# Kernel optimization log

Hardware: AMD Instinct MI355X
Metric: run time of the kernel (lower is better)

Reference implementation:

```python
import jax, jax.numpy as jnp
import numpy as np

EMBED_DIM = 2048
NUM_HEADS = 16
HEAD_DIM = EMBED_DIM // NUM_HEADS


def setup_inputs() -> dict:
    key = jax.random.key(0)
    ks = jax.random.split(key, 9)
    s = 1.0 / np.sqrt(EMBED_DIM)
    x = jax.random.normal(ks[0], (2, 2048, EMBED_DIM), dtype=jnp.float32)
    Wq = jax.random.uniform(ks[1], (EMBED_DIM, EMBED_DIM), jnp.float32, -s, s)
    bq = jax.random.uniform(ks[2], (EMBED_DIM,), jnp.float32, -s, s)
    Wk = jax.random.uniform(ks[3], (EMBED_DIM, EMBED_DIM), jnp.float32, -s, s)
    bk = jax.random.uniform(ks[4], (EMBED_DIM,), jnp.float32, -s, s)
    Wv = jax.random.uniform(ks[5], (EMBED_DIM, EMBED_DIM), jnp.float32, -s, s)
    bv = jax.random.uniform(ks[6], (EMBED_DIM,), jnp.float32, -s, s)
    Wo = jax.random.uniform(ks[7], (EMBED_DIM, EMBED_DIM), jnp.float32, -s, s)
    bo = jax.random.uniform(ks[8], (EMBED_DIM,), jnp.float32, -s, s)
    return {"x": x, "Wq": Wq, "bq": bq, "Wk": Wk, "bk": bk,
            "Wv": Wv, "bv": bv, "Wo": Wo, "bo": bo}


def reference(x, Wq, bq, Wk, bk, Wv, bv, Wo, bo):
    B, S, E = x.shape
    H, D = NUM_HEADS, HEAD_DIM
    # projections (torch Linear: y = x @ W.T + b)
    def proj(W, b):
        return (x @ W.T + b).reshape(B, S, H, D).transpose(0, 2, 1, 3)  # [B,H,S,D]
    q, k, v = proj(Wq, bq), proj(Wk, bk), proj(Wv, bv)
    scores = jnp.einsum('bhqd,bhkd->bhqk', q, k) / np.sqrt(D).astype(np.float32)
    causal = jnp.triu(jnp.ones((S, S), dtype=bool), k=1)
    scores = jnp.where(causal, jnp.float32(-1e9), scores)
    attn = jax.nn.softmax(scores, axis=-1)
    ctx = jnp.einsum('bhqk,bhkd->bhqd', attn, v)
    ctx = ctx.transpose(0, 2, 1, 3).reshape(B, S, E)
    return ctx @ Wo.T + bo
```

## Files before the change

### kernel.cpp

```cpp
#include <hip/hip_runtime.h>
#include <hip/hip_bf16.h>

typedef __bf16 bf16_t;
typedef bf16_t bf16x8 __attribute__((ext_vector_type(8)));
typedef float f32x4 __attribute__((ext_vector_type(4)));

__device__ __forceinline__ f32x4 mfma16(bf16x8 a, bf16x8 b, f32x4 c) {
    return __builtin_amdgcn_mfma_f32_16x16x32_bf16(a, b, c, 0, 0, 0);
}

__device__ __forceinline__ void load16_to_lds(const void* g, void* l) {
    __builtin_amdgcn_global_load_lds(
        (__attribute__((address_space(1))) unsigned int*)g,
        (__attribute__((address_space(3))) unsigned int*)l, 16, 0, 0);
}

__device__ __forceinline__ bf16x8 cvt8(f32x4 a, f32x4 b) {
    bf16x8 r;
    r[0] = (bf16_t)a[0]; r[1] = (bf16_t)a[1]; r[2] = (bf16_t)a[2]; r[3] = (bf16_t)a[3];
    r[4] = (bf16_t)b[0]; r[5] = (bf16_t)b[1]; r[6] = (bf16_t)b[2]; r[7] = (bf16_t)b[3];
    return r;
}

__global__ __launch_bounds__(256)
void cvt_bf16(const float* __restrict__ in, bf16_t* __restrict__ out) {
    const long i = ((long)blockIdx.x * 256 + threadIdx.x) * 8;
    *(bf16x8*)(out + i) = cvt8(*(const f32x4*)(in + i), *(const f32x4*)(in + i + 4));
}

__global__ __launch_bounds__(256)
void cvt_all(const float* __restrict__ x,
             const float* __restrict__ Wq, const float* __restrict__ Wk, const float* __restrict__ Wv,
             bf16_t* __restrict__ xb, bf16_t* __restrict__ wqb,
             bf16_t* __restrict__ wkb, bf16_t* __restrict__ wvb) {
    const long NW = 4194304;
    const int y = blockIdx.y;
    const float* s; bf16_t* o;
    if      (y == 0) { s = x;      o = xb;      }
    else if (y == 1) { s = x + NW; o = xb + NW; }
    else if (y == 2) { s = Wq;     o = wqb;     }
    else if (y == 3) { s = Wk;     o = wkb;     }
    else             { s = Wv;     o = wvb;     }
    const long i = ((long)blockIdx.x * 256 + threadIdx.x) * 8;
    *(bf16x8*)(o + i) = cvt8(*(const f32x4*)(s + i), *(const f32x4*)(s + i + 4));
}

__global__ __launch_bounds__(256)
void gemm_qkv(const bf16_t* __restrict__ X,
              const bf16_t* __restrict__ W0, const bf16_t* __restrict__ W1, const bf16_t* __restrict__ W2,
              const float* __restrict__ B0, const float* __restrict__ B1, const float* __restrict__ B2,
              bf16_t* __restrict__ O0, bf16_t* __restrict__ O1, bf16_t* __restrict__ O2)
{
    __shared__ __align__(16) bf16_t As[128 * 32];
    __shared__ __align__(16) bf16_t Bs[128 * 32];
    const int z = blockIdx.z;
    const bf16_t* W = (z == 0) ? W0 : (z == 1 ? W1 : W2);
    const float* Bv = (z == 0) ? B0 : (z == 1 ? B1 : B2);
    bf16_t* O       = (z == 0) ? O0 : (z == 1 ? O1 : O2);

    const int tid = threadIdx.x;
    const int w = tid >> 6, l = tid & 63;
    const int lm = l & 15, lq = l >> 4;
    const long arow0 = (long)blockIdx.y * 128;
    const long brow0 = (long)blockIdx.x * 128;
    const int wm = (w >> 1) * 64, wn = (w & 1) * 64;

    f32x4 acc[4][4] = {};

    for (int kt = 0; kt < 2048; kt += 32) {
#pragma unroll
        for (int i = 0; i < 2; ++i) {
            const int c = w * 128 + i * 64 + l;
            const int row = c >> 2, ce = (c & 3) * 8;
            load16_to_lds(X + (arow0 + row) * 2048 + kt + ce, As + (w * 2 + i) * 512);
            load16_to_lds(W + (brow0 + row) * 2048 + kt + ce, Bs + (w * 2 + i) * 512);
        }
        __syncthreads();
        bf16x8 af[4], bfr[4];
#pragma unroll
        for (int i = 0; i < 4; ++i)
            af[i] = *(const bf16x8*)(As + (wm + i * 16 + lm) * 32 + lq * 8);
#pragma unroll
        for (int j = 0; j < 4; ++j)
            bfr[j] = *(const bf16x8*)(Bs + (wn + j * 16 + lm) * 32 + lq * 8);
#pragma unroll
        for (int i = 0; i < 4; ++i)
#pragma unroll
            for (int j = 0; j < 4; ++j)
                acc[i][j] = mfma16(af[i], bfr[j], acc[i][j]);
        __syncthreads();
    }

    const float scale = (z == 0) ? 0.08838834764831845f : 1.0f;
#pragma unroll
    for (int j = 0; j < 4; ++j) {
        const int col = (int)brow0 + wn + j * 16 + lm;
        const float bb = Bv[col];
        const int h = col >> 7, d = col & 127;
#pragma unroll
        for (int i = 0; i < 4; ++i) {
            const int rbase = (int)arow0 + wm + i * 16 + lq * 4;
#pragma unroll
            for (int r = 0; r < 4; ++r) {
                const int row = rbase + r;
                const int b = row >> 11, s = row & 2047;
                const float v = (acc[i][j][r] + bb) * scale;
                long idx;
                if (z == 2) idx = ((long)(b * 16 + h) * 128 + d) * 2048 + s;
                else        idx = ((long)(b * 16 + h) * 2048 + s) * 128 + d;
                O[idx] = (bf16_t)v;
            }
        }
    }
}

__global__ __launch_bounds__(256)
void gemm_out(const bf16_t* __restrict__ A, const bf16_t* __restrict__ W,
              const float* __restrict__ Bv, float* __restrict__ O)
{
    __shared__ __align__(16) bf16_t As[128 * 32];
    __shared__ __align__(16) bf16_t Bs[128 * 32];

    const int tid = threadIdx.x;
    const int w = tid >> 6, l = tid & 63;
    const int lm = l & 15, lq = l >> 4;
    const long arow0 = (long)blockIdx.y * 128;
    const long brow0 = (long)blockIdx.x * 128;
    const int wm = (w >> 1) * 64, wn = (w & 1) * 64;

    f32x4 acc[4][4] = {};

    for (int kt = 0; kt < 2048; kt += 32) {
#pragma unroll
        for (int i = 0; i < 2; ++i) {
            const int c = w * 128 + i * 64 + l;
            const int row = c >> 2, ce = (c & 3) * 8;
            load16_to_lds(A + (arow0 + row) * 2048 + kt + ce, As + (w * 2 + i) * 512);
            load16_to_lds(W + (brow0 + row) * 2048 + kt + ce, Bs + (w * 2 + i) * 512);
        }
        __syncthreads();
        bf16x8 af[4], bfr[4];
#pragma unroll
        for (int i = 0; i < 4; ++i)
            af[i] = *(const bf16x8*)(As + (wm + i * 16 + lm) * 32 + lq * 8);
#pragma unroll
        for (int j = 0; j < 4; ++j)
            bfr[j] = *(const bf16x8*)(Bs + (wn + j * 16 + lm) * 32 + lq * 8);
#pragma unroll
        for (int i = 0; i < 4; ++i)
#pragma unroll
            for (int j = 0; j < 4; ++j)
                acc[i][j] = mfma16(af[i], bfr[j], acc[i][j]);
        __syncthreads();
    }

#pragma unroll
    for (int j = 0; j < 4; ++j) {
        const int col = (int)brow0 + wn + j * 16 + lm;
        const float bb = Bv[col];
#pragma unroll
        for (int i = 0; i < 4; ++i) {
            const int rbase = (int)arow0 + wm + i * 16 + lq * 4;
#pragma unroll
            for (int r = 0; r < 4; ++r)
                O[(long)(rbase + r) * 2048 + col] = acc[i][j][r] + bb;
        }
    }
}

__global__ __launch_bounds__(256, 4)
void attn(const bf16_t* __restrict__ Q, const bf16_t* __restrict__ K,
          const bf16_t* __restrict__ VT, bf16_t* __restrict__ CTX)
{
    __shared__ __align__(16) bf16_t Ks[64 * 128];
    __shared__ __align__(16) bf16_t Vs[128 * 64];
    __shared__ __align__(16) bf16_t Ps[4][16 * 64];

    const int tid = threadIdx.x;
    const int w = tid >> 6, l = tid & 63;
    const int lm = l & 15, lq = l >> 4;

    const int flat = blockIdx.x;
    const int g = flat >> 8, i0 = flat & 255;
    const int bh = i0 >> 3, j = i0 & 7;
    const int qx = (g == 0) ? j : (g == 1) ? (15 - j) : (g == 2) ? (16 + j) : (31 - j);

    const int q0 = qx * 64;
    const int qw = q0 + w * 16;
    const long base = (long)bh * 2048 * 128;

    bf16x8 qf[4];
#pragma unroll
    for (int ks = 0; ks < 4; ++ks)
        qf[ks] = *(const bf16x8*)(Q + base + (long)(qw + lm) * 128 + ks * 32 + lq * 8);

    f32x4 ctx[8] = {};
    float mrow[4], lrow[4];
#pragma unroll
    for (int r = 0; r < 4; ++r) { mrow[r] = -1e30f; lrow[r] = 0.f; }

    const int ntiles = qx + 1;
    for (int it = 0; it < ntiles; ++it) {
        const int s0 = it << 6;
        __syncthreads();
#pragma unroll
        for (int i = 0; i < 4; ++i) {
            const int s = (w * 4 + i) * 64 + l;
            const int kk = s >> 4, dcs = s & 15;
            const int dc = dcs ^ (kk & 15);
            load16_to_lds(K + base + (long)(s0 + kk) * 128 + dc * 8, Ks + (w * 4 + i) * 512);
            const int d = s >> 3, cs = s & 7;
            const int c = cs ^ (d & 7);
            load16_to_lds(VT + base + (long)d * 2048 + s0 + c * 8, Vs + (w * 4 + i) * 512);
        }
        __syncthreads();

        f32x4 sc[4] = {};
#pragma unroll
        for (int ks = 0; ks < 4; ++ks)
#pragma unroll
            for (int kj = 0; kj < 4; ++kj) {
                const int kk = kj * 16 + lm;
                const int dc = ks * 4 + lq;
                const bf16x8 kf = *(const bf16x8*)(Ks + (kk * 16 + (dc ^ (kk & 15))) * 8);
                sc[kj] = mfma16(qf[ks], kf, sc[kj]);
            }
        if (s0 + 63 > qw) {
#pragma unroll
            for (int kj = 0; kj < 4; ++kj) {
                const int colg = s0 + kj * 16 + lm;
#pragma unroll
                for (int r = 0; r < 4; ++r) {
                    const int rowg = qw + lq * 4 + r;
                    if (colg > rowg) sc[kj][r] = -1e30f;
                }
            }
        }
#pragma unroll
        for (int r = 0; r < 4; ++r) {
            float mx = fmaxf(fmaxf(sc[0][r], sc[1][r]), fmaxf(sc[2][r], sc[3][r]));
#pragma unroll
            for (int off = 1; off < 16; off <<= 1)
                mx = fmaxf(mx, __shfl_xor(mx, off, 64));
            const float mn = fmaxf(mrow[r], mx);
            const float alpha = exp2f((mrow[r] - mn) * 1.4426950408889634f);
            mrow[r] = mn;
            float sum = 0.f;
#pragma unroll
            for (int kj = 0; kj < 4; ++kj) {
                const float p = exp2f((sc[kj][r] - mn) * 1.4426950408889634f);
                sc[kj][r] = p;
                sum += p;
            }
#pragma unroll
            for (int off = 1; off < 16; off <<= 1)
                sum += __shfl_xor(sum, off, 64);
            lrow[r] = lrow[r] * alpha + sum;
#pragma unroll
            for (int dj = 0; dj < 8; ++dj)
                ctx[dj][r] *= alpha;
        }
#pragma unroll
        for (int kj = 0; kj < 4; ++kj)
#pragma unroll
            for (int r = 0; r < 4; ++r) {
                const int q = lq * 4 + r;
                const int kk = kj * 16 + lm;
                Ps[w][q * 64 + ((kk >> 3) ^ (q & 7)) * 8 + (kk & 7)] = (bf16_t)sc[kj][r];
            }
        __syncthreads();
#pragma unroll
        for (int ks2 = 0; ks2 < 2; ++ks2) {
            const int c = ks2 * 4 + lq;
            const bf16x8 pf = *(const bf16x8*)(&Ps[w][0] + lm * 64 + (c ^ (lm & 7)) * 8);
#pragma unroll
            for (int dj = 0; dj < 8; ++dj) {
                const int d = dj * 16 + lm;
                const bf16x8 vf = *(const bf16x8*)(Vs + (d * 8 + (c ^ (d & 7))) * 8);
                ctx[dj] = mfma16(pf, vf, ctx[dj]);
            }
        }
    }

    const int b = bh >> 4, h = bh & 15;
#pragma unroll
    for (int r = 0; r < 4; ++r) {
        const float inv = 1.0f / lrow[r];
        const int s = qw + lq * 4 + r;
#pragma unroll
        for (int dj = 0; dj < 8; ++dj) {
            const int e = h * 128 + dj * 16 + lm;
            CTX[((long)(b * 2048 + s)) * 2048 + e] = (bf16_t)(ctx[dj][r] * inv);
        }
    }
}

extern "C" void kernel_launch(void* const* d_in, const int* in_sizes, int n_in,
                              void* d_out, int out_size, void* d_ws, size_t ws_size,
                              hipStream_t stream)
{
    const float* x  = (const float*)d_in[0];
    const float* Wq = (const float*)d_in[1];
    const float* bq = (const float*)d_in[2];
    const float* Wk = (const float*)d_in[3];
    const float* bk = (const float*)d_in[4];
    const float* Wv = (const float*)d_in[5];
    const float* bv = (const float*)d_in[6];
    const float* Wo = (const float*)d_in[7];
    const float* bo = (const float*)d_in[8];
    float* out = (float*)d_out;

    const size_t NTOK = (size_t)2 * 2048 * 2048;
    const size_t NW   = (size_t)2048 * 2048;
    bf16_t* q  = (bf16_t*)d_ws;
    bf16_t* k  = q  + NTOK;
    bf16_t* vT = k  + NTOK;
    bf16_t* cx = vT + NTOK;
    bf16_t* xb  = cx;
    bf16_t* wob = q;
    bf16_t* wqb = (bf16_t*)d_out;
    bf16_t* wkb = wqb + NW;
    bf16_t* wvb = wkb + NW;

    dim3 blk(256);
    cvt_all<<<dim3(2048, 5), blk, 0, stream>>>(x, Wq, Wk, Wv, xb, wqb, wkb, wvb);
    gemm_qkv<<<dim3(16, 32, 3), blk, 0, stream>>>(xb, wqb, wkb, wvb, bq, bk, bv, q, k, vT);
    attn<<<dim3(1024), blk, 0, stream>>>(q, k, vT, cx);
    cvt_bf16<<<dim3(2048), blk, 0, stream>>>(Wo, wob);
    gemm_out<<<dim3(16, 32), blk, 0, stream>>>(cx, wob, bo, out);
}
```

Baseline: 496.6 us.

## Register-prefetch next K/V tile, reorder blocks longest-first, drop P barrier

Result: slower. 660.5 us (+33.0%).

```diff
diff --git a/kernel.cpp b/kernel.cpp
--- a/kernel.cpp
+++ b/kernel.cpp
@@ -181,9 +181,8 @@
     const int lm = l & 15, lq = l >> 4;
 
     const int flat = blockIdx.x;
-    const int g = flat >> 8, i0 = flat & 255;
-    const int bh = i0 >> 3, j = i0 & 7;
-    const int qx = (g == 0) ? j : (g == 1) ? (15 - j) : (g == 2) ? (16 + j) : (31 - j);
+    const int qx = 31 - (flat >> 5);
+    const int bh = flat & 31;
 
     const int q0 = qx * 64;
     const int qw = q0 + w * 16;
@@ -199,6 +198,16 @@
 #pragma unroll
     for (int r = 0; r < 4; ++r) { mrow[r] = -1e30f; lrow[r] = 0.f; }
 
+    bf16x8 rk[4], rv[4];
+#pragma unroll
+    for (int i = 0; i < 4; ++i) {
+        const int s = (w * 4 + i) * 64 + l;
+        const int kk = s >> 4, dc = (s & 15) ^ (kk & 15);
+        rk[i] = *(const bf16x8*)(K + base + (long)kk * 128 + dc * 8);
+        const int d = s >> 3, c = (s & 7) ^ (d & 7);
+        rv[i] = *(const bf16x8*)(VT + base + (long)d * 2048 + c * 8);
+    }
+
     const int ntiles = qx + 1;
     for (int it = 0; it < ntiles; ++it) {
         const int s0 = it << 6;
@@ -206,14 +215,21 @@
 #pragma unroll
         for (int i = 0; i < 4; ++i) {
             const int s = (w * 4 + i) * 64 + l;
-            const int kk = s >> 4, dcs = s & 15;
-            const int dc = dcs ^ (kk & 15);
-            load16_to_lds(K + base + (long)(s0 + kk) * 128 + dc * 8, Ks + (w * 4 + i) * 512);
-            const int d = s >> 3, cs = s & 7;
-            const int c = cs ^ (d & 7);
-            load16_to_lds(VT + base + (long)d * 2048 + s0 + c * 8, Vs + (w * 4 + i) * 512);
-        }
-        __syncthreads();
+            *(bf16x8*)(Ks + s * 8) = rk[i];
+            *(bf16x8*)(Vs + s * 8) = rv[i];
+        }
+        __syncthreads();
+        if (it + 1 < ntiles) {
+            const int s0n = s0 + 64;
+#pragma unroll
+            for (int i = 0; i < 4; ++i) {
+                const int s = (w * 4 + i) * 64 + l;
+                const int kk = s >> 4, dc = (s & 15) ^ (kk & 15);
+                rk[i] = *(const bf16x8*)(K + base + (long)(s0n + kk) * 128 + dc * 8);
+                const int d = s >> 3, c = (s & 7) ^ (d & 7);
+                rv[i] = *(const bf16x8*)(VT + base + (long)d * 2048 + s0n + c * 8);
+            }
+        }
 
         f32x4 sc[4] = {};
 #pragma unroll
@@ -268,7 +284,7 @@
                 const int kk = kj * 16 + lm;
                 Ps[w][q * 64 + ((kk >> 3) ^ (q & 7)) * 8 + (kk & 7)] = (bf16_t)sc[kj][r];
             }
-        __syncthreads();
+        __asm__ volatile("s_waitcnt lgkmcnt(0)" ::: "memory");
 #pragma unroll
         for (int ks2 = 0; ks2 < 2; ++ks2) {
             const int c = ks2 * 4 + lq;
```
